# Performance work log

Hardware: AMD Instinct MI355X
Metric: run time of the kernel (lower is better)

Reference implementation:

```python
import jax, jax.numpy as jnp
import numpy as np

H, HKV, HD = 16, 16, 64  # num_heads, num_kv_heads, head_dim

def rotate_half(x):
    x1, x2 = jnp.split(x, 2, axis=-1)
    return jnp.concatenate((-x2, x1), axis=-1)

def setup_inputs() -> dict:
    key = jax.random.key(0)
    ks = jax.random.split(key, 4)
    B, L, D = 4, 2048, 1024
    hidden_states = jax.random.normal(ks[0], (B, L, D), jnp.float32)
    # RoPE tables [L, head_dim]
    inv_freq = 1.0 / (10000.0 ** (jnp.arange(0, HD, 2, dtype=jnp.float32) / HD))
    freqs = jnp.outer(jnp.arange(L, dtype=jnp.float32), inv_freq)
    emb = jnp.concatenate((freqs, freqs), axis=-1)
    cos, sin = jnp.cos(emb), jnp.sin(emb)
    active_mask = jax.random.randint(ks[1], (B, L), 0, 2).astype(bool)
    Wqkv = jax.random.normal(ks[2], ((H + 2 * HKV) * HD, D), jnp.float32) / np.sqrt(D)
    Wo = jax.random.normal(ks[3], (D, H * HD), jnp.float32) / np.sqrt(H * HD)
    return {"hidden_states": hidden_states, "cos": cos, "sin": sin,
            "active_mask": active_mask, "Wqkv": Wqkv, "Wo": Wo}

def reference(hidden_states, cos, sin, active_mask, Wqkv, Wo):
    B, L, D = hidden_states.shape
    qkv = (hidden_states @ Wqkv.T).reshape(B, L, H + 2 * HKV, HD)
    q = qkv[:, :, :H]
    k = qkv[:, :, H:H + HKV]
    v = qkv[:, :, H + HKV:]
    c = cos[:, None, :]  # [L,1,HD] broadcasts over B and heads
    s = sin[:, None, :]
    q = q * c + rotate_half(q) * s
    k = k * c + rotate_half(k) * s
    # sparse queries: only active positions emit queries
    q = q * active_mask[:, :, None, None].astype(q.dtype)
    scale = 1.0 / np.sqrt(HD)
    scores = jnp.einsum('bqhd,bkhd->bhqk', q, k) * scale  # [B,H,L,L]
    attn = jax.nn.softmax(scores, axis=-1)
    out = jnp.einsum('bhqk,bkhd->bqhd', attn, v).reshape(B, L, H * HD)
    out = out @ Wo.T
    return out * active_mask[:, :, None].astype(out.dtype)
```

## Files before the change

### kernel.cpp

```cpp
#include <hip/hip_runtime.h>
#include <cstdint>

typedef _Float16 f16;
typedef __attribute__((ext_vector_type(2))) __fp16 fp16v2;
typedef __attribute__((ext_vector_type(4))) _Float16 f16x4;
typedef __attribute__((ext_vector_type(8))) _Float16 f16x8;
typedef __attribute__((ext_vector_type(4))) float f32x4;
typedef __attribute__((ext_vector_type(16))) float f32x16;

#if __has_builtin(__builtin_amdgcn_exp2f)
#define EXP2F(x) __builtin_amdgcn_exp2f(x)
#else
#define EXP2F(x) exp2f(x)
#endif

#if __has_builtin(__builtin_amdgcn_fdot2)
#define FDOT2(a, b, c) __builtin_amdgcn_fdot2((a), (b), (c), false)
#else
#define FDOT2(a, b, c) ((c) + (float)(a)[0] * (float)(b)[0] + (float)(a)[1] * (float)(b)[1])
#endif

#define GLOAD_LDS16(gp, lp) \
  __builtin_amdgcn_global_load_lds((const __attribute__((address_space(1))) void*)(gp), \
                                   (__attribute__((address_space(3))) void*)(lp), 16, 0, 0)


__global__ __launch_bounds__(256) void cvt_all(const float4* __restrict__ h, f16x4* __restrict__ h16,
                                               const float4* __restrict__ wq, f16x4* __restrict__ wq16,
                                               const float4* __restrict__ wo, f16x4* __restrict__ wo16,
                                               const float* __restrict__ cosb, const float* __restrict__ sinb,
                                               float2* __restrict__ cst) {
  int i = blockIdx.x * 256 + threadIdx.x;
  if (i >= 3145728) {
    const int i2 = i - 3145728;
    const int d = i2 >> 11, l = i2 & 2047;
    cst[i2] = make_float2(cosb[l * 64 + d], sinb[l * 64 + d]);
    return;
  }
  const float4* src;
  f16x4* dst;
  if (i < 2097152) { src = h + i; dst = h16 + i; }
  else if (i < 2883584) { src = wq + (i - 2097152); dst = wq16 + (i - 2097152); }
  else { src = wo + (i - 2883584); dst = wo16 + (i - 2883584); }
  float4 v = *src;
  f16x4 o;
  o.x = (f16)v.x; o.y = (f16)v.y; o.z = (f16)v.z; o.w = (f16)v.w;
  *dst = o;
}

template<int EPI, int N, int K>
__global__ __launch_bounds__(256) void gemm_bt(
    const f16* __restrict__ A, const f16* __restrict__ Bm,
    f16* __restrict__ Qf, f16* __restrict__ Kf, f16* __restrict__ Vf,
    float* __restrict__ Cout, const int* __restrict__ mask,
    const float2* __restrict__ cst) {
  constexpr int NT = N / 128;
  const int bm = blockIdx.x / NT;
  const int bn = blockIdx.x % NT;
  const int lane = threadIdx.x & 63;
  const int wid  = threadIdx.x >> 6;
  const int wm = wid >> 1, wn = wid & 1;

  __shared__ f16 sA[128 * 32];
  __shared__ f16 sB[128 * 32];

  f32x4 acc[4][4] = {};

  const f16* Abase = A + (size_t)bm * 128 * K;
  const f16* Bbase = Bm + (size_t)bn * 128 * K;
  const int srow = lane >> 2;
  const int skk  = ((lane & 3) ^ ((lane >> 3) & 3)) * 8;

  const int lo = lane & 15;
  const int h16 = lane >> 4;
  const int xr = (lo >> 1) & 3;

#define GEMM_STAGE(k0)                                                        \
  do {                                                                        \
    __syncthreads();                                                          \
    _Pragma("unroll")                                                         \
    for (int c = 0; c < 2; ++c) {                                             \
      const int chunk = wid * 2 + c;                                          \
      GLOAD_LDS16(Abase + (chunk * 16 + srow) * K + (k0) + skk, &sA[chunk * 512]); \
      GLOAD_LDS16(Bbase + (chunk * 16 + srow) * K + (k0) + skk, &sB[chunk * 512]); \
    }                                                                         \
    __syncthreads();                                                          \
    _Pragma("unroll")                                                         \
    for (int i = 0; i < 4; ++i) {                                             \
      af[i] = *(const f16x8*)&sA[(wm * 64 + i * 16 + lo) * 32 + (h16 ^ xr) * 8]; \
      bf[i] = *(const f16x8*)&sB[(wn * 64 + i * 16 + lo) * 32 + (h16 ^ xr) * 8]; \
    }                                                                         \
  } while (0)

  const bool swp = (EPI == 1) && (bn < 16);
  if (swp) {
    for (int k0 = 0; k0 < K; k0 += 32) {
      f16x8 af[4], bf[4];
      GEMM_STAGE(k0);
      #pragma unroll
      for (int i = 0; i < 4; ++i)
        #pragma unroll
        for (int j = 0; j < 4; ++j)
          acc[i][j] = __builtin_amdgcn_mfma_f32_16x16x32_f16(bf[i], af[j], acc[i][j], 0, 0, 0);
    }
  } else {
    for (int k0 = 0; k0 < K; k0 += 32) {
      f16x8 af[4], bf[4];
      GEMM_STAGE(k0);
      #pragma unroll
      for (int i = 0; i < 4; ++i)
        #pragma unroll
        for (int j = 0; j < 4; ++j)
          acc[i][j] = __builtin_amdgcn_mfma_f32_16x16x32_f16(af[i], bf[j], acc[i][j], 0, 0, 0);
    }
  }

  if constexpr (EPI == 1) {
    const int head = bn * 2 + wn;
    if (head < 32) {
      f16* dst = (head < 16) ? Qf : Kf;
      const int h15 = head & 15;
      const int bb = bm >> 4;
      const int llbase = (bm & 15) * 128 + wm * 64;
      const int ahi = h16 >> 1, kkl = h16 & 1;
      f16* base = dst + (size_t)(bb * 16 + h15) * 64 * 2048;
      #pragma unroll
      for (int j = 0; j < 4; ++j) {
        const int ll = llbase + j * 16 + lo;
        float msc = 1.0f;
        if (head < 16) msc = mask[bb * 2048 + ll] ? 0.18033688011112042f : 0.0f;
        union { f16x8 v; fp16v2 hh[4]; } u0, u1;
        #pragma unroll
        for (int i = 0; i < 2; ++i) {
          float y0[4], y1[4];
          #pragma unroll
          for (int r = 0; r < 4; ++r) {
            const float2 cs = cst[(size_t)(i * 16 + 4 * h16 + r) * 2048 + ll];
            const float xl = acc[i][j][r], xh = acc[i + 2][j][r];
            y0[r] = (xl * cs.x - xh * cs.y) * msc;
            y1[r] = (xh * cs.x + xl * cs.y) * msc;
          }
          u0.hh[i * 2 + 0] = __builtin_amdgcn_cvt_pkrtz(y0[0], y0[1]);
          u0.hh[i * 2 + 1] = __builtin_amdgcn_cvt_pkrtz(y0[2], y0[3]);
          u1.hh[i * 2 + 0] = __builtin_amdgcn_cvt_pkrtz(y1[0], y1[1]);
          u1.hh[i * 2 + 1] = __builtin_amdgcn_cvt_pkrtz(y1[2], y1[3]);
        }
        const int t = ll >> 5, q5 = ll & 31;
        f16* p = base + (size_t)t * 2048 + (ahi * 32 + q5) * 8;
        *(f16x8*)(p + (kkl + 0) * 512) = u0.v;
        *(f16x8*)(p + (kkl + 2) * 512) = u1.v;
      }
    } else {
      const int hv = head - 32;
      #pragma unroll
      for (int i = 0; i < 4; ++i) {
        #pragma unroll
        for (int j = 0; j < 4; ++j) {
          #pragma unroll
          for (int r = 0; r < 4; ++r) {
            const int gm = bm * 128 + wm * 64 + i * 16 + (lane >> 4) * 4 + r;
            const int bb = gm >> 11, ll = gm & 2047;
            const int dd = j * 16 + lo;
            const int k = ll & 31;
            const int i32 = (k & ~12) | ((k & 4) << 1) | ((k & 8) >> 1);
            const int cc = i32 >> 4, hih = (i32 >> 3) & 1, jj = i32 & 7;
            const int blk = dd >> 5, qq = dd & 31;
            Vf[((size_t)(bb * 16 + hv) * 64 + (ll >> 5)) * 2048 +
               (cc * 2 + blk) * 512 + hih * 256 + qq * 8 + jj] = (f16)acc[i][j][r];
          }
        }
      }
    }
  } else {
    #pragma unroll
    for (int i = 0; i < 4; ++i) {
      #pragma unroll
      for (int j = 0; j < 4; ++j) {
        #pragma unroll
        for (int r = 0; r < 4; ++r) {
          const int gm = bm * 128 + wm * 64 + i * 16 + (lane >> 4) * 4 + r;
          const int gn = bn * 128 + wn * 64 + j * 16 + lo;
          const float mv = mask[gm] ? 1.0f : 0.0f;
          Cout[(size_t)gm * 1024 + gn] = acc[i][j][r] * mv;
        }
      }
    }
  }
#undef GEMM_STAGE
}

#define LOADKV(kd, vd, kp, vp)                       \
  do {                                               \
    _Pragma("unroll")                                \
    for (int _i = 0; _i < 4; ++_i) {                 \
      kd[_i] = *(const f16x8*)&(kp)[_i * 512];       \
      vd[_i] = *(const f16x8*)&(vp)[_i * 512];       \
    }                                                \
  } while (0)

#define ATTN_BODY64(kr, vr)                                                      \
  do {                                                                           \
    f32x16 sa = {}, sb = {};                                                     \
    __builtin_amdgcn_s_setprio(1);                                               \
    _Pragma("unroll")                                                            \
    for (int _k = 0; _k < 4; ++_k)                                               \
      sa = __builtin_amdgcn_mfma_f32_32x32x16_f16(kr[_k], qfa[_k], sa, 0, 0, 0); \
    _Pragma("unroll")                                                            \
    for (int _k = 0; _k < 4; ++_k)                                               \
      sb = __builtin_amdgcn_mfma_f32_32x32x16_f16(kr[_k], qfb[_k], sb, 0, 0, 0); \
    __builtin_amdgcn_s_setprio(0);                                               \
    union PU { fp16v2 h[4]; f16x8 v; } pa0, pa1, pb0, pb1;                       \
    _Pragma("unroll")                                                            \
    for (int _i = 0; _i < 4; ++_i) {                                             \
      pa0.h[_i] = __builtin_amdgcn_cvt_pkrtz(EXP2F(sa[2 * _i]), EXP2F(sa[2 * _i + 1]));       \
      pa1.h[_i] = __builtin_amdgcn_cvt_pkrtz(EXP2F(sa[8 + 2 * _i]), EXP2F(sa[8 + 2 * _i + 1])); \
      la = FDOT2(pa0.h[_i], kOne, la);                                           \
      la = FDOT2(pa1.h[_i], kOne, la);                                           \
    }                                                                            \
    _Pragma("unroll")                                                            \
    for (int _i = 0; _i < 4; ++_i) {                                             \
      pb0.h[_i] = __builtin_amdgcn_cvt_pkrtz(EXP2F(sb[2 * _i]), EXP2F(sb[2 * _i + 1]));       \
      pb1.h[_i] = __builtin_amdgcn_cvt_pkrtz(EXP2F(sb[8 + 2 * _i]), EXP2F(sb[8 + 2 * _i + 1])); \
      lb = FDOT2(pb0.h[_i], kOne, lb);                                           \
      lb = FDOT2(pb1.h[_i], kOne, lb);                                           \
    }                                                                            \
    __builtin_amdgcn_s_setprio(1);                                               \
    oa0 = __builtin_amdgcn_mfma_f32_32x32x16_f16(vr[0], pa0.v, oa0, 0, 0, 0);    \
    oa1 = __builtin_amdgcn_mfma_f32_32x32x16_f16(vr[1], pa0.v, oa1, 0, 0, 0);    \
    ob0 = __builtin_amdgcn_mfma_f32_32x32x16_f16(vr[0], pb0.v, ob0, 0, 0, 0);    \
    ob1 = __builtin_amdgcn_mfma_f32_32x32x16_f16(vr[1], pb0.v, ob1, 0, 0, 0);    \
    oa0 = __builtin_amdgcn_mfma_f32_32x32x16_f16(vr[2], pa1.v, oa0, 0, 0, 0);    \
    oa1 = __builtin_amdgcn_mfma_f32_32x32x16_f16(vr[3], pa1.v, oa1, 0, 0, 0);    \
    ob0 = __builtin_amdgcn_mfma_f32_32x32x16_f16(vr[2], pb1.v, ob0, 0, 0, 0);    \
    ob1 = __builtin_amdgcn_mfma_f32_32x32x16_f16(vr[3], pb1.v, ob1, 0, 0, 0);    \
    __builtin_amdgcn_s_setprio(0);                                               \
  } while (0)

__global__ __launch_bounds__(512) void attn_kernel(const f16* __restrict__ Qf,
                                                   const f16* __restrict__ Kf,
                                                   const f16* __restrict__ Vf,
                                                   f16* __restrict__ Ow) {
  const int bid = (blockIdx.x & 7) * 64 + (blockIdx.x >> 3);
  const int bh = bid >> 3;
  const int qt = bid & 7;
  const int lane = threadIdx.x & 63;
  const int wid = threadIdx.x >> 6;
  const int qw = wid & 3;
  const int kvh = wid >> 2;
  const int hi = lane >> 5;
  const int q = lane & 31;

  __shared__ float o_lds[8][32][65];
  __shared__ float l_lds[8][32];

  const f16* Qb = Qf + (size_t)bh * 64 * 2048;
  const f16* Kb = Kf + (size_t)bh * 64 * 2048;
  const f16* Vb = Vf + (size_t)bh * 64 * 2048;

  const int ta = qt * 8 + qw * 2;
  f16x8 qfa[4], qfb[4];
  {
    const f16* pa = Qb + (size_t)ta * 2048 + lane * 8;
    const f16* pb = pa + 2048;
    #pragma unroll
    for (int kk = 0; kk < 4; ++kk) {
      qfa[kk] = *(const f16x8*)&pa[kk * 512];
      qfb[kk] = *(const f16x8*)&pb[kk * 512];
    }
  }

  f32x16 oa0 = {}, oa1 = {}, ob0 = {}, ob1 = {};
  float la = 0.0f, lb = 0.0f;
  const fp16v2 kOne = {(__fp16)1.0f, (__fp16)1.0f};

  const f16* kptr = Kb + (size_t)(kvh * 32) * 2048 + lane * 8;
  const f16* vptr = Vb + (size_t)(kvh * 32) * 2048 + lane * 8;
  f16x8 ka[4], va[4], kn[4], vn[4];
  LOADKV(ka, va, kptr, vptr);
  for (int t = 0; t < 32; t += 2) {
    LOADKV(kn, vn, kptr + 2048, vptr + 2048);
    ATTN_BODY64(ka, va);
    if (t + 2 < 32)
      LOADKV(ka, va, kptr + 4096, vptr + 4096);
    ATTN_BODY64(kn, vn);
    kptr += 4096; vptr += 4096;
  }

  float lha = la + __shfl_xor(la, 32, 64);
  float lhb = lb + __shfl_xor(lb, 32, 64);

  if (kvh == 1) {
    #pragma unroll
    for (int blk = 0; blk < 2; ++blk)
      #pragma unroll
      for (int g = 0; g < 4; ++g)
        #pragma unroll
        for (int j = 0; j < 4; ++j) {
          const int d = blk * 32 + g * 8 + 4 * hi + j;
          o_lds[qw * 2 + 0][q][d] = blk ? oa1[g * 4 + j] : oa0[g * 4 + j];
          o_lds[qw * 2 + 1][q][d] = blk ? ob1[g * 4 + j] : ob0[g * 4 + j];
        }
    if (hi == 0) { l_lds[qw * 2 + 0][q] = lha; l_lds[qw * 2 + 1][q] = lhb; }
  }
  __syncthreads();
  if (kvh == 0) {
    const float inva = 1.0f / (lha + l_lds[qw * 2 + 0][q]);
    const float invb = 1.0f / (lhb + l_lds[qw * 2 + 1][q]);
    const int b = bh >> 4, h = bh & 15;
    const int qra = qt * 256 + qw * 64 + q;
    f16* orowa = Ow + ((size_t)(b * 2048 + qra)) * 1024 + h * 64;
    f16* orowb = orowa + 32 * 1024;
    #pragma unroll
    for (int blk = 0; blk < 2; ++blk) {
      #pragma unroll
      for (int g = 0; g < 4; ++g) {
        f16x4 sta, stb;
        #pragma unroll
        for (int j = 0; j < 4; ++j) {
          const int d = blk * 32 + g * 8 + 4 * hi + j;
          sta[j] = (f16)(((blk ? oa1[g * 4 + j] : oa0[g * 4 + j]) + o_lds[qw * 2 + 0][q][d]) * inva);
          stb[j] = (f16)(((blk ? ob1[g * 4 + j] : ob0[g * 4 + j]) + o_lds[qw * 2 + 1][q][d]) * invb);
        }
        *(f16x4*)&orowa[blk * 32 + g * 8 + 4 * hi] = sta;
        *(f16x4*)&orowb[blk * 32 + g * 8 + 4 * hi] = stb;
      }
    }
  }
}

extern "C" void kernel_launch(void* const* d_in, const int* in_sizes, int n_in,
                              void* d_out, int out_size, void* d_ws, size_t ws_size,
                              hipStream_t stream) {
  const float* hidden = (const float*)d_in[0];
  const float* cosb   = (const float*)d_in[1];
  const float* sinb   = (const float*)d_in[2];
  const int*   mask   = (const int*)d_in[3];
  const float* wqkv   = (const float*)d_in[4];
  const float* wo     = (const float*)d_in[5];
  float* out = (float*)d_out;
  char* ws = (char*)d_ws;

  f16* h16    = (f16*)(ws + 0);
  f16* wqkv16 = (f16*)(ws + 16777216);
  f16* wo16   = (f16*)(ws + 23068672);
  f16* Qfb    = (f16*)(ws + 25165824);
  f16* Kfb    = (f16*)(ws + 41943040);
  f16* Vfb    = (f16*)(ws + 58720256);
  float2* cst = (float2*)(ws + 75497472);
  f16* Ow     = h16;

  cvt_all<<<12544, 256, 0, stream>>>((const float4*)hidden, (f16x4*)h16,
                                     (const float4*)wqkv, (f16x4*)wqkv16,
                                     (const float4*)wo, (f16x4*)wo16,
                                     cosb, sinb, cst);

  gemm_bt<1, 3072, 1024><<<64 * 24, 256, 0, stream>>>(h16, wqkv16, Qfb, Kfb, Vfb,
                                                      nullptr, mask, cst);

  attn_kernel<<<512, 512, 0, stream>>>(Qfb, Kfb, Vfb, Ow);

  gemm_bt<2, 1024, 1024><<<64 * 8, 256, 0, stream>>>(Ow, wo16, nullptr, nullptr, nullptr,
                                                     out, mask, nullptr);
}
```

Before: 188.4 us.

## Double-buffer GEMM k-tiles with larger 256x128 blocks and XCD-aware block swizzle

Replaces the single-buffered 128x128 GEMM with a 512-thread, 256x128-tile kernel using K=64 tiles held in two LDS buffers. Global-to-LDS loads for tile k+2 are issued while MFMAs on the current tile run, with explicit vmcnt waits, barriers and setprio to overlap memory and compute. It also remaps block indices so neighbouring tiles land on the same XCD for cache reuse. The cost is more LDS per block (96 KB), which lowers occupancy, and more complex manual synchronisation.

Result: faster. 162.8 us (-13.6%).

```diff
diff --git a/kernel.cpp b/kernel.cpp
--- a/kernel.cpp
+++ b/kernel.cpp
@@ -23,7 +23,6 @@
 #define GLOAD_LDS16(gp, lp) \
   __builtin_amdgcn_global_load_lds((const __attribute__((address_space(1))) void*)(gp), \
                                    (__attribute__((address_space(3))) void*)(lp), 16, 0, 0)
-
 
 __global__ __launch_bounds__(256) void cvt_all(const float4* __restrict__ h, f16x4* __restrict__ h16,
                                                const float4* __restrict__ wq, f16x4* __restrict__ wq16,
@@ -49,93 +48,123 @@
 }
 
 template<int EPI, int N, int K>
-__global__ __launch_bounds__(256) void gemm_bt(
+__global__ __launch_bounds__(512) void gemm_bt2(
     const f16* __restrict__ A, const f16* __restrict__ Bm,
     f16* __restrict__ Qf, f16* __restrict__ Kf, f16* __restrict__ Vf,
     float* __restrict__ Cout, const int* __restrict__ mask,
     const float2* __restrict__ cst) {
   constexpr int NT = N / 128;
-  const int bm = blockIdx.x / NT;
-  const int bn = blockIdx.x % NT;
-  const int lane = threadIdx.x & 63;
-  const int wid  = threadIdx.x >> 6;
-  const int wm = wid >> 1, wn = wid & 1;
-
-  __shared__ f16 sA[128 * 32];
-  __shared__ f16 sB[128 * 32];
+  constexpr int NKT = K / 64;
+  const int tid = threadIdx.x;
+  const int lane = tid & 63;
+  const int wid = tid >> 6;
+  const int wm = wid >> 1;
+  const int wn = wid & 1;
+
+  constexpr int nwg = 32 * NT;
+  constexpr int cpx = nwg >> 3;
+  const int swz = (blockIdx.x & 7) * cpx + (blockIdx.x >> 3);
+  const int bm = swz / NT;
+  const int bn = swz % NT;
+
+  __shared__ f16 sA[2][256 * 64];
+  __shared__ f16 sB[2][128 * 64];
+
+  const f16* Abase = A + (size_t)bm * 256 * K;
+  const f16* Bbase = Bm + (size_t)bn * 128 * K;
 
   f32x4 acc[4][4] = {};
-
-  const f16* Abase = A + (size_t)bm * 128 * K;
-  const f16* Bbase = Bm + (size_t)bn * 128 * K;
-  const int srow = lane >> 2;
-  const int skk  = ((lane & 3) ^ ((lane >> 3) & 3)) * 8;
+  f16x8 af[4][2], bf[4][2];
+
+  const int rowt = tid >> 3;
+  const int c8 = (tid & 7) ^ (rowt & 7);
+  const bool swp = (EPI == 1) && (bn < 16);
+
+#define STAGE_KT(SLOT, KT)                                                      \
+  do {                                                                          \
+    _Pragma("unroll")                                                           \
+    for (int g = 0; g < 4; ++g)                                                 \
+      GLOAD_LDS16(Abase + (size_t)(g * 64 + rowt) * K + (KT) * 64 + c8 * 8,     \
+                  &sA[SLOT][g * 4096 + tid * 8]);                               \
+    _Pragma("unroll")                                                           \
+    for (int g = 0; g < 2; ++g)                                                 \
+      GLOAD_LDS16(Bbase + (size_t)(g * 64 + rowt) * K + (KT) * 64 + c8 * 8,     \
+                  &sB[SLOT][g * 4096 + tid * 8]);                               \
+  } while (0)
+
+#define MFMA_CLUSTER(KS)                                                        \
+  do {                                                                          \
+    __builtin_amdgcn_s_setprio(1);                                              \
+    if (swp) {                                                                  \
+      _Pragma("unroll")                                                         \
+      for (int i = 0; i < 4; ++i)                                               \
+        _Pragma("unroll")                                                       \
+        for (int j = 0; j < 4; ++j)                                             \
+          acc[i][j] = __builtin_amdgcn_mfma_f32_16x16x32_f16(bf[i][KS], af[j][KS], acc[i][j], 0, 0, 0); \
+    } else {                                                                    \
+      _Pragma("unroll")                                                         \
+      for (int i = 0; i < 4; ++i)                                               \
+        _Pragma("unroll")                                                       \
+        for (int j = 0; j < 4; ++j)                                             \
+          acc[i][j] = __builtin_amdgcn_mfma_f32_16x16x32_f16(af[i][KS], bf[j][KS], acc[i][j], 0, 0, 0); \
+    }                                                                           \
+    __builtin_amdgcn_s_setprio(0);                                              \
+  } while (0)
+
+#define KTILE(VMC, DOSTAGE, KT, SLOT)                                           \
+  do {                                                                          \
+    asm volatile("s_waitcnt vmcnt(" #VMC ")" ::: "memory");                     \
+    __builtin_amdgcn_s_barrier();                                               \
+    __builtin_amdgcn_sched_barrier(0);                                          \
+    _Pragma("unroll")                                                           \
+    for (int i = 0; i < 4; ++i) {                                               \
+      _Pragma("unroll")                                                         \
+      for (int ks = 0; ks < 2; ++ks) {                                          \
+        af[i][ks] = *(const f16x8*)&sA[SLOT][(wm * 64 + i * 16 + (lane & 15)) * 64 + ((ks * 4 + (lane >> 4)) ^ (lane & 7)) * 8]; \
+        bf[i][ks] = *(const f16x8*)&sB[SLOT][(wn * 64 + i * 16 + (lane & 15)) * 64 + ((ks * 4 + (lane >> 4)) ^ (lane & 7)) * 8]; \
+      }                                                                         \
+    }                                                                           \
+    MFMA_CLUSTER(0);                                                            \
+    asm volatile("s_waitcnt lgkmcnt(0)" ::: "memory");                          \
+    __builtin_amdgcn_sched_barrier(0);                                          \
+    __builtin_amdgcn_s_barrier();                                               \
+    if (DOSTAGE) { STAGE_KT(SLOT, (KT) + 2); }                                  \
+    __builtin_amdgcn_sched_barrier(0);                                          \
+    MFMA_CLUSTER(1);                                                            \
+  } while (0)
+
+  STAGE_KT(0, 0);
+  STAGE_KT(1, 1);
+#pragma unroll 1
+  for (int it = 0; it < NKT - 2; it += 2) {
+    KTILE(6, true, it, 0);
+    KTILE(6, true, it + 1, 1);
+  }
+  KTILE(6, false, NKT - 2, 0);
+  KTILE(0, false, NKT - 1, 1);
 
   const int lo = lane & 15;
-  const int h16 = lane >> 4;
-  const int xr = (lo >> 1) & 3;
-
-#define GEMM_STAGE(k0)                                                        \
-  do {                                                                        \
-    __syncthreads();                                                          \
-    _Pragma("unroll")                                                         \
-    for (int c = 0; c < 2; ++c) {                                             \
-      const int chunk = wid * 2 + c;                                          \
-      GLOAD_LDS16(Abase + (chunk * 16 + srow) * K + (k0) + skk, &sA[chunk * 512]); \
-      GLOAD_LDS16(Bbase + (chunk * 16 + srow) * K + (k0) + skk, &sB[chunk * 512]); \
-    }                                                                         \
-    __syncthreads();                                                          \
-    _Pragma("unroll")                                                         \
-    for (int i = 0; i < 4; ++i) {                                             \
-      af[i] = *(const f16x8*)&sA[(wm * 64 + i * 16 + lo) * 32 + (h16 ^ xr) * 8]; \
-      bf[i] = *(const f16x8*)&sB[(wn * 64 + i * 16 + lo) * 32 + (h16 ^ xr) * 8]; \
-    }                                                                         \
-  } while (0)
-
-  const bool swp = (EPI == 1) && (bn < 16);
-  if (swp) {
-    for (int k0 = 0; k0 < K; k0 += 32) {
-      f16x8 af[4], bf[4];
-      GEMM_STAGE(k0);
-      #pragma unroll
-      for (int i = 0; i < 4; ++i)
-        #pragma unroll
-        for (int j = 0; j < 4; ++j)
-          acc[i][j] = __builtin_amdgcn_mfma_f32_16x16x32_f16(bf[i], af[j], acc[i][j], 0, 0, 0);
-    }
-  } else {
-    for (int k0 = 0; k0 < K; k0 += 32) {
-      f16x8 af[4], bf[4];
-      GEMM_STAGE(k0);
-      #pragma unroll
-      for (int i = 0; i < 4; ++i)
-        #pragma unroll
-        for (int j = 0; j < 4; ++j)
-          acc[i][j] = __builtin_amdgcn_mfma_f32_16x16x32_f16(af[i], bf[j], acc[i][j], 0, 0, 0);
-    }
-  }
-
   if constexpr (EPI == 1) {
     const int head = bn * 2 + wn;
     if (head < 32) {
       f16* dst = (head < 16) ? Qf : Kf;
       const int h15 = head & 15;
-      const int bb = bm >> 4;
-      const int llbase = (bm & 15) * 128 + wm * 64;
-      const int ahi = h16 >> 1, kkl = h16 & 1;
-      f16* base = dst + (size_t)(bb * 16 + h15) * 64 * 2048;
+      const int h16l = lane >> 4;
+      const int ahi = h16l >> 1, kkl = h16l & 1;
       #pragma unroll
       for (int j = 0; j < 4; ++j) {
-        const int ll = llbase + j * 16 + lo;
+        const int grow = bm * 256 + wm * 64 + j * 16 + lo;
+        const int bb = grow >> 11, ll = grow & 2047;
         float msc = 1.0f;
         if (head < 16) msc = mask[bb * 2048 + ll] ? 0.18033688011112042f : 0.0f;
+        f16* base = dst + (size_t)(bb * 16 + h15) * 64 * 2048;
         union { f16x8 v; fp16v2 hh[4]; } u0, u1;
         #pragma unroll
         for (int i = 0; i < 2; ++i) {
           float y0[4], y1[4];
           #pragma unroll
           for (int r = 0; r < 4; ++r) {
-            const float2 cs = cst[(size_t)(i * 16 + 4 * h16 + r) * 2048 + ll];
+            const float2 cs = cst[(size_t)(i * 16 + 4 * h16l + r) * 2048 + ll];
             const float xl = acc[i][j][r], xh = acc[i + 2][j][r];
             y0[r] = (xl * cs.x - xh * cs.y) * msc;
             y1[r] = (xh * cs.x + xl * cs.y) * msc;
@@ -158,7 +187,7 @@
         for (int j = 0; j < 4; ++j) {
           #pragma unroll
           for (int r = 0; r < 4; ++r) {
-            const int gm = bm * 128 + wm * 64 + i * 16 + (lane >> 4) * 4 + r;
+            const int gm = bm * 256 + wm * 64 + i * 16 + (lane >> 4) * 4 + r;
             const int bb = gm >> 11, ll = gm & 2047;
             const int dd = j * 16 + lo;
             const int k = ll & 31;
@@ -178,7 +207,7 @@
       for (int j = 0; j < 4; ++j) {
         #pragma unroll
         for (int r = 0; r < 4; ++r) {
-          const int gm = bm * 128 + wm * 64 + i * 16 + (lane >> 4) * 4 + r;
+          const int gm = bm * 256 + wm * 64 + i * 16 + (lane >> 4) * 4 + r;
           const int gn = bn * 128 + wn * 64 + j * 16 + lo;
           const float mv = mask[gm] ? 1.0f : 0.0f;
           Cout[(size_t)gm * 1024 + gn] = acc[i][j][r] * mv;
@@ -186,7 +215,9 @@
       }
     }
   }
-#undef GEMM_STAGE
+#undef KTILE
+#undef MFMA_CLUSTER
+#undef STAGE_KT
 }
 
 #define LOADKV(kd, vd, kp, vp)                       \
@@ -354,11 +385,11 @@
                                      (const float4*)wo, (f16x4*)wo16,
                                      cosb, sinb, cst);
 
-  gemm_bt<1, 3072, 1024><<<64 * 24, 256, 0, stream>>>(h16, wqkv16, Qfb, Kfb, Vfb,
-                                                      nullptr, mask, cst);
+  gemm_bt2<1, 3072, 1024><<<768, 512, 0, stream>>>(h16, wqkv16, Qfb, Kfb, Vfb,
+                                                   nullptr, mask, cst);
 
   attn_kernel<<<512, 512, 0, stream>>>(Qfb, Kfb, Vfb, Ow);
 
-  gemm_bt<2, 1024, 1024><<<64 * 8, 256, 0, stream>>>(Ow, wo16, nullptr, nullptr, nullptr,
-                                                     out, mask, nullptr);
+  gemm_bt2<2, 1024, 1024><<<256, 512, 0, stream>>>(Ow, wo16, nullptr, nullptr, nullptr,
+                                                   out, mask, nullptr);
 }
```
